# Kernel optimization log

Measured on AMD Instinct MI355X. Metric: run time of the kernel, lower is better.

Reference implementation:

```python
import jax, jax.numpy as jnp
import numpy as np
import math

B, L, C, H = 2, 2048, 768, 12
D = C // H
MAX_SCALE_MUL = math.log(100.0)


def setup_inputs() -> dict:
    key = jax.random.key(0)
    ks = jax.random.split(key, 8)
    std = 0.02
    x = jax.random.normal(ks[0], (B, L, C), dtype=jnp.float32)
    attn_bias = jax.random.normal(ks[1], (1, 1, L, L), dtype=jnp.float32)
    W_qkv = jax.random.normal(ks[2], (3 * C, C), dtype=jnp.float32) * std
    b_qkv = jnp.zeros((3 * C,), dtype=jnp.float32)
    # attn_l2_norm=True: learned per-head log-scale, init log(4)
    scale_mul_log = jnp.full((1, H, 1, 1), math.log(4.0), dtype=jnp.float32)
    W_proj = jax.random.normal(ks[3], (C, C), dtype=jnp.float32) * std
    b_proj = jnp.zeros((C,), dtype=jnp.float32)
    return {"x": x, "attn_bias": attn_bias, "W_qkv": W_qkv, "b_qkv": b_qkv,
            "scale_mul_log": scale_mul_log, "W_proj": W_proj, "b_proj": b_proj}


def _l2norm(t):
    # matches F.normalize(dim=-1, eps=1e-12)
    n = jnp.sqrt(jnp.sum(t * t, axis=-1, keepdims=True))
    return t / jnp.maximum(n, 1e-12)


def reference(x, attn_bias, W_qkv, b_qkv, scale_mul_log, W_proj, b_proj):
    Bx, Lx, Cx = x.shape
    qkv = (x @ W_qkv.T + b_qkv).reshape(Bx, Lx, 3, H, D)
    # -> [3, B, H, L, D]
    qkv = jnp.transpose(qkv, (2, 0, 3, 1, 4))
    q, k, v = qkv[0], qkv[1], qkv[2]
    scale_mul = jnp.exp(jnp.minimum(scale_mul_log, MAX_SCALE_MUL))  # [1,H,1,1]
    q = _l2norm(q) * scale_mul
    k = _l2norm(k)
    # scale = 1 in the l2-norm branch
    attn = jnp.einsum('bhqd,bhkd->bhqk', q, k) + attn_bias
    attn = jax.nn.softmax(attn, axis=-1)
    oup = jnp.einsum('bhqk,bhkd->bhqd', attn, v)          # [B,H,L,D]
    oup = jnp.transpose(oup, (0, 2, 1, 3)).reshape(Bx, Lx, Cx)
    return oup @ W_proj.T + b_proj
```

## Files before the change

kernel.cpp:

```cpp
#include <hip/hip_runtime.h>
#include <math.h>

#define B_ 2
#define L_ 2048
#define C_ 768
#define H_ 12
#define D_ 64
#define M_ (B_ * L_)
#define MAXLOG 4.605170185988091f

typedef __bf16 bf16;
typedef __bf16 bf16x4 __attribute__((ext_vector_type(4)));
typedef __bf16 bf16x8 __attribute__((ext_vector_type(8)));
typedef float  f32x4  __attribute__((ext_vector_type(4)));
typedef short  s16x4  __attribute__((ext_vector_type(4)));

#define SZ_  ((size_t)B_ * H_ * L_ * D_)
#define MC_  ((size_t)M_ * C_)
#define WQ_  ((size_t)3 * C_ * C_)
#define WP_  ((size_t)C_ * C_)

static __device__ __forceinline__ f32x4 mfma16(bf16x4 a, bf16x4 b, f32x4 c) {
#if __has_builtin(__builtin_amdgcn_mfma_f32_16x16x16_bf16)
    return __builtin_amdgcn_mfma_f32_16x16x16_bf16(a, b, c, 0, 0, 0);
#elif __has_builtin(__builtin_amdgcn_mfma_f32_16x16x16bf16_1k)
    return __builtin_amdgcn_mfma_f32_16x16x16bf16_1k(*(s16x4*)&a, *(s16x4*)&b, c, 0, 0, 0);
#else
    f32x4 d;
    asm("v_mfma_f32_16x16x16_bf16 %0, %1, %2, %3" : "=v"(d) : "v"(a), "v"(b), "v"(c));
    return d;
#endif
}

__global__ __launch_bounds__(256) void prep(
    const float4* __restrict__ x, const float4* __restrict__ Wq,
    const float4* __restrict__ Wp,
    bf16* __restrict__ xb, bf16* __restrict__ wqb,
    bf16* __restrict__ Wh, bf16* __restrict__ Wl)
{
    const int X4 = (int)(MC_ / 4);
    const int W4 = (int)(WQ_ / 4);
    const int S4 = (int)(WP_ / 4);
    const int total = X4 + W4 + S4;

    const int i0 = blockIdx.x * 256 + threadIdx.x;
    const int stride = gridDim.x * 256;
    for (int i = i0; i < total; i += stride) {
        if (i < X4) {
            const float4 v = x[i];
            bf16x4 o; o[0]=(bf16)v.x; o[1]=(bf16)v.y; o[2]=(bf16)v.z; o[3]=(bf16)v.w;
            *(bf16x4*)&xb[(size_t)i * 4] = o;
        } else if (i < X4 + W4) {
            const int j = i - X4;
            const float4 v = Wq[j];
            bf16x4 o; o[0]=(bf16)v.x; o[1]=(bf16)v.y; o[2]=(bf16)v.z; o[3]=(bf16)v.w;
            *(bf16x4*)&wqb[(size_t)j * 4] = o;
        } else {
            const int j = i - X4 - W4;
            const float4 v = Wp[j];
            bf16x4 h, l;
            h[0]=(bf16)v.x; l[0]=(bf16)(v.x-(float)h[0]);
            h[1]=(bf16)v.y; l[1]=(bf16)(v.y-(float)h[1]);
            h[2]=(bf16)v.z; l[2]=(bf16)(v.z-(float)h[2]);
            h[3]=(bf16)v.w; l[3]=(bf16)(v.w-(float)h[3]);
            *(bf16x4*)&Wh[(size_t)j * 4] = h;
            *(bf16x4*)&Wl[(size_t)j * 4] = l;
        }
    }
}

__global__ __launch_bounds__(256) void qkv_mfma(
    const bf16* __restrict__ A, const bf16* __restrict__ W,
    const float* __restrict__ bias, const float* __restrict__ sml,
    bf16* __restrict__ qb, bf16* __restrict__ kb, bf16* __restrict__ vtb)
{
    __shared__ __align__(16) bf16 As[128][72];
    __shared__ __align__(16) bf16 Bs[64][72];

    const int t    = threadIdx.x;
    const int w    = t >> 6;
    const int lane = t & 63;
    const int quad = lane >> 4;
    const int c    = lane & 15;
    const int m0   = blockIdx.x * 128;
    const int n0   = blockIdx.y * 64;

    const int r0 = t >> 3;
    const int cg = (t & 7) * 8;

    f32x4 acc[2][4];
    #pragma unroll
    for (int mt = 0; mt < 2; ++mt)
        #pragma unroll
        for (int nt = 0; nt < 4; ++nt) acc[mt][nt] = (f32x4){0.f,0.f,0.f,0.f};

    bf16x8 areg[4], breg[2];
    #pragma unroll
    for (int p = 0; p < 4; ++p)
        areg[p] = *(const bf16x8*)&A[(size_t)(m0 + r0 + 32 * p) * C_ + cg];
    #pragma unroll
    for (int p = 0; p < 2; ++p)
        breg[p] = *(const bf16x8*)&W[(size_t)(n0 + r0 + 32 * p) * C_ + cg];

    for (int kt = 0; kt < C_; kt += 64) {
        __syncthreads();
        #pragma unroll
        for (int p = 0; p < 4; ++p) *(bf16x8*)&As[r0 + 32 * p][cg] = areg[p];
        #pragma unroll
        for (int p = 0; p < 2; ++p) *(bf16x8*)&Bs[r0 + 32 * p][cg] = breg[p];

        const int kt2 = kt + 64;
        if (kt2 < C_) {
            #pragma unroll
            for (int p = 0; p < 4; ++p)
                areg[p] = *(const bf16x8*)&A[(size_t)(m0 + r0 + 32 * p) * C_ + kt2 + cg];
            #pragma unroll
            for (int p = 0; p < 2; ++p)
                breg[p] = *(const bf16x8*)&W[(size_t)(n0 + r0 + 32 * p) * C_ + kt2 + cg];
        }
        __syncthreads();

        #pragma unroll
        for (int ks = 0; ks < 2; ++ks) {
            #pragma unroll
            for (int mt = 0; mt < 2; ++mt) {
                const bf16x8 a = *(const bf16x8*)&As[w * 32 + mt * 16 + c][ks * 32 + quad * 8];
                #pragma unroll
                for (int nt = 0; nt < 4; ++nt) {
                    const bf16x8 b = *(const bf16x8*)&Bs[nt * 16 + c][ks * 32 + quad * 8];
                    acc[mt][nt] = __builtin_amdgcn_mfma_f32_16x16x32_bf16(a, b, acc[mt][nt], 0, 0, 0);
                }
            }
        }
    }

    const int three = blockIdx.y / H_;
    const int h     = blockIdx.y % H_;
    const int bidx  = m0 >> 11;
    const int l0    = (m0 & (L_ - 1)) + w * 32;

    if (three < 2) {
        bf16* dst = (three == 0) ? qb : kb;
        const float scale = (three == 0) ? expf(fminf(sml[h], MAXLOG)) : 1.0f;
        #pragma unroll
        for (int mt = 0; mt < 2; ++mt) {
            float val[4][4];
            float ss[4] = {0.f, 0.f, 0.f, 0.f};
            #pragma unroll
            for (int nt = 0; nt < 4; ++nt) {
                const float bb = bias[n0 + nt * 16 + c];
                #pragma unroll
                for (int reg = 0; reg < 4; ++reg) {
                    const float v = acc[mt][nt][reg] + bb;
                    val[nt][reg] = v;
                    ss[reg] += v * v;
                }
            }
            #pragma unroll
            for (int reg = 0; reg < 4; ++reg) {
                float s = ss[reg];
                #pragma unroll
                for (int off = 1; off < 16; off <<= 1) s += __shfl_xor(s, off, 16);
                const float inv = scale / fmaxf(sqrtf(s), 1e-12f);
                const int l = l0 + mt * 16 + quad * 4 + reg;
                #pragma unroll
                for (int nt = 0; nt < 4; ++nt)
                    dst[((size_t)(bidx * H_ + h) * L_ + l) * D_ + nt * 16 + c] =
                        (bf16)(val[nt][reg] * inv);
            }
        }
    } else {
        #pragma unroll
        for (int mt = 0; mt < 2; ++mt)
            #pragma unroll
            for (int nt = 0; nt < 4; ++nt) {
                const int d = nt * 16 + c;
                const float bb = bias[n0 + d];
                const int l = l0 + mt * 16 + quad * 4;
                bf16x4 o;
                #pragma unroll
                for (int reg = 0; reg < 4; ++reg) o[reg] = (bf16)(acc[mt][nt][reg] + bb);
                *(bf16x4*)&vtb[((size_t)(bidx * H_ + h) * D_ + d) * L_ + l] = o;
            }
    }
}

__global__ __launch_bounds__(256, 3) void flash_mfma(
    const bf16* __restrict__ q, const bf16* __restrict__ k,
    const bf16* __restrict__ vt, const float* __restrict__ bias,
    const float* __restrict__ sml,
    bf16* __restrict__ aoh, bf16* __restrict__ aol)
{
    __shared__ __align__(16) bf16 Ks0 [64][72];
    __shared__ __align__(16) bf16 Vts0[64][72];
    __shared__ __align__(16) bf16 Ks1 [64][72];
    __shared__ __align__(16) bf16 Vts1[64][72];

    const int t    = threadIdx.x;
    const int w    = t >> 6;
    const int lane = t & 63;
    const int quad = lane >> 4;
    const int c    = lane & 15;
    const int q0   = blockIdx.x * 64;
    const int bh   = blockIdx.y;
    const int h    = bh % H_;
    const int b    = bh / H_;
    const size_t base  = (size_t)bh * L_ * D_;
    const size_t vbase = (size_t)bh * D_ * L_;
    const int qrow = q0 + w * 16 + c;

    const float FMAX = expf(fminf(sml[h], MAXLOG)) + 8.0f;

    bf16x8 qf[2];
    qf[0] = *(const bf16x8*)&q[base + (size_t)qrow * D_ + quad * 8];
    qf[1] = *(const bf16x8*)&q[base + (size_t)qrow * D_ + 32 + quad * 8];

    const int r0  = t >> 3,         c00 = (t & 7) * 8;
    const int r1  = (t + 256) >> 3, c01 = ((t + 256) & 7) * 8;

    float l_acc = 0.f;
    f32x4 o[4];
    #pragma unroll
    for (int dt = 0; dt < 4; ++dt) o[dt] = (f32x4){0.f, 0.f, 0.f, 0.f};

    bf16x8 kreg[2], vreg[2];
    f32x4  bregA[4], bregB[4];

    kreg[0] = *(const bf16x8*)&k [base  + (size_t)r0 * D_ + c00];
    kreg[1] = *(const bf16x8*)&k [base  + (size_t)r1 * D_ + c01];
    vreg[0] = *(const bf16x8*)&vt[vbase + (size_t)r0 * L_ + c00];
    vreg[1] = *(const bf16x8*)&vt[vbase + (size_t)r1 * L_ + c01];
    #pragma unroll
    for (int s = 0; s < 4; ++s)
        bregA[s] = *(const f32x4*)&bias[(size_t)qrow * L_ + 16 * s + 4 * quad];

    *(bf16x8*)&Ks0 [r0][c00] = kreg[0];
    *(bf16x8*)&Ks0 [r1][c01] = kreg[1];
    *(bf16x8*)&Vts0[r0][c00] = vreg[0];
    *(bf16x8*)&Vts0[r1][c01] = vreg[1];

    kreg[0] = *(const bf16x8*)&k [base  + (size_t)(64 + r0) * D_ + c00];
    kreg[1] = *(const bf16x8*)&k [base  + (size_t)(64 + r1) * D_ + c01];
    vreg[0] = *(const bf16x8*)&vt[vbase + (size_t)r0 * L_ + 64 + c00];
    vreg[1] = *(const bf16x8*)&vt[vbase + (size_t)r1 * L_ + 64 + c01];
    #pragma unroll
    for (int s = 0; s < 4; ++s)
        bregB[s] = *(const f32x4*)&bias[(size_t)qrow * L_ + 64 + 16 * s + 4 * quad];
    __syncthreads();

#define FSTEP(KS_C, VT_C, KS_N, VT_N, BC, IT) do {                               \
    if ((IT) + 1 < 32) {                                                         \
        *(bf16x8*)&KS_N [r0][c00] = kreg[0];                                     \
        *(bf16x8*)&KS_N [r1][c01] = kreg[1];                                     \
        *(bf16x8*)&VT_N [r0][c00] = vreg[0];                                     \
        *(bf16x8*)&VT_N [r1][c01] = vreg[1];                                     \
    }                                                                            \
    f32x4 st[4];                                                                 \
    _Pragma("unroll") for (int s = 0; s < 4; ++s) st[s] = BC[s];                 \
    if ((IT) + 2 < 32) {                                                         \
        const int kp = ((IT) + 2) * 64;                                          \
        kreg[0] = *(const bf16x8*)&k [base  + (size_t)(kp + r0) * D_ + c00];     \
        kreg[1] = *(const bf16x8*)&k [base  + (size_t)(kp + r1) * D_ + c01];     \
        vreg[0] = *(const bf16x8*)&vt[vbase + (size_t)r0 * L_ + kp + c00];       \
        vreg[1] = *(const bf16x8*)&vt[vbase + (size_t)r1 * L_ + kp + c01];       \
        _Pragma("unroll") for (int s = 0; s < 4; ++s)                            \
            BC[s] = *(const f32x4*)&bias[(size_t)qrow * L_ + kp + 16*s + 4*quad];\
    }                                                                            \
    _Pragma("unroll") for (int ks = 0; ks < 2; ++ks)                             \
        _Pragma("unroll") for (int s = 0; s < 4; ++s) {                          \
            const bf16x8 kf = *(const bf16x8*)&KS_C[s*16 + c][ks*32 + quad*8];   \
            st[s] = __builtin_amdgcn_mfma_f32_16x16x32_bf16(kf, qf[ks], st[s], 0, 0, 0); \
        }                                                                        \
    bf16x4 pf[4];                                                                \
    _Pragma("unroll") for (int s = 0; s < 4; ++s)                                \
        _Pragma("unroll") for (int r = 0; r < 4; ++r) {                          \
            const float pv = __expf(st[s][r] - FMAX);                            \
            l_acc += pv;                                                         \
            pf[s][r] = (bf16)pv;                                                 \
        }                                                                        \
    _Pragma("unroll") for (int s = 0; s < 4; ++s)                                \
        _Pragma("unroll") for (int dt = 0; dt < 4; ++dt) {                       \
            const bf16x4 vfr = *(const bf16x4*)&VT_C[dt*16 + c][16*s + 4*quad];  \
            o[dt] = mfma16(vfr, pf[s], o[dt]);                                   \
        }                                                                        \
    __syncthreads();                                                             \
} while (0)

    for (int it = 0; it < 32; it += 2) {
        FSTEP(Ks0, Vts0, Ks1, Vts1, bregA, it);
        FSTEP(Ks1, Vts1, Ks0, Vts0, bregB, it + 1);
    }
#undef FSTEP

    float rs = l_acc;
    rs += __shfl_xor(rs, 16);
    rs += __shfl_xor(rs, 32);
    const float linv = 1.0f / rs;

    const size_t obase = ((size_t)(b * L_ + qrow)) * C_ + h * 64;
    #pragma unroll
    for (int dt = 0; dt < 4; ++dt) {
        bf16x4 hv, lv;
        #pragma unroll
        for (int r = 0; r < 4; ++r) {
            const float v = o[dt][r] * linv;
            hv[r] = (bf16)v;
            lv[r] = (bf16)(v - (float)hv[r]);
        }
        *(bf16x4*)&aoh[obase + dt * 16 + 4 * quad] = hv;
        *(bf16x4*)&aol[obase + dt * 16 + 4 * quad] = lv;
    }
}

__global__ __launch_bounds__(256) void proj_mfma(
    const bf16* __restrict__ Ahg, const bf16* __restrict__ Alg,
    const bf16* __restrict__ Whg, const bf16* __restrict__ Wlg,
    const float* __restrict__ bias, float* __restrict__ outp)
{
    __shared__ __align__(16) bf16 Ah[64][72];
    __shared__ __align__(16) bf16 Al[64][72];
    __shared__ __align__(16) bf16 Bh[64][72];
    __shared__ __align__(16) bf16 Bl[64][72];

    const int t    = threadIdx.x;
    const int w    = t >> 6;
    const int lane = t & 63;
    const int quad = lane >> 4;
    const int c    = lane & 15;
    const int m0   = blockIdx.x * 64;
    const int n0   = blockIdx.y * 64;

    const int r0 = t >> 3;
    const int cg = (t & 7) * 8;

    f32x4 acc[4];
    #pragma unroll
    for (int nt = 0; nt < 4; ++nt) acc[nt] = (f32x4){0.f,0.f,0.f,0.f};

    bf16x8 ahreg[2], alreg[2], bhreg[2], blreg[2];
    #pragma unroll
    for (int p = 0; p < 2; ++p) {
        ahreg[p] = *(const bf16x8*)&Ahg[(size_t)(m0 + r0 + 32 * p) * C_ + cg];
        alreg[p] = *(const bf16x8*)&Alg[(size_t)(m0 + r0 + 32 * p) * C_ + cg];
        bhreg[p] = *(const bf16x8*)&Whg[(size_t)(n0 + r0 + 32 * p) * C_ + cg];
        blreg[p] = *(const bf16x8*)&Wlg[(size_t)(n0 + r0 + 32 * p) * C_ + cg];
    }

    for (int kt = 0; kt < C_; kt += 64) {
        __syncthreads();
        #pragma unroll
        for (int p = 0; p < 2; ++p) {
            *(bf16x8*)&Ah[r0 + 32 * p][cg] = ahreg[p];
            *(bf16x8*)&Al[r0 + 32 * p][cg] = alreg[p];
            *(bf16x8*)&Bh[r0 + 32 * p][cg] = bhreg[p];
            *(bf16x8*)&Bl[r0 + 32 * p][cg] = blreg[p];
        }

        const int kt2 = kt + 64;
        if (kt2 < C_) {
            #pragma unroll
            for (int p = 0; p < 2; ++p) {
                ahreg[p] = *(const bf16x8*)&Ahg[(size_t)(m0 + r0 + 32 * p) * C_ + kt2 + cg];
                alreg[p] = *(const bf16x8*)&Alg[(size_t)(m0 + r0 + 32 * p) * C_ + kt2 + cg];
                bhreg[p] = *(const bf16x8*)&Whg[(size_t)(n0 + r0 + 32 * p) * C_ + kt2 + cg];
                blreg[p] = *(const bf16x8*)&Wlg[(size_t)(n0 + r0 + 32 * p) * C_ + kt2 + cg];
            }
        }
        __syncthreads();

        #pragma unroll
        for (int ks = 0; ks < 2; ++ks) {
            const bf16x8 ah = *(const bf16x8*)&Ah[w * 16 + c][ks * 32 + quad * 8];
            const bf16x8 al = *(const bf16x8*)&Al[w * 16 + c][ks * 32 + quad * 8];
            #pragma unroll
            for (int nt = 0; nt < 4; ++nt) {
                const bf16x8 bh = *(const bf16x8*)&Bh[nt * 16 + c][ks * 32 + quad * 8];
                const bf16x8 bl = *(const bf16x8*)&Bl[nt * 16 + c][ks * 32 + quad * 8];
                acc[nt] = __builtin_amdgcn_mfma_f32_16x16x32_bf16(ah, bh, acc[nt], 0, 0, 0);
                acc[nt] = __builtin_amdgcn_mfma_f32_16x16x32_bf16(ah, bl, acc[nt], 0, 0, 0);
                acc[nt] = __builtin_amdgcn_mfma_f32_16x16x32_bf16(al, bh, acc[nt], 0, 0, 0);
            }
        }
    }

    #pragma unroll
    for (int nt = 0; nt < 4; ++nt) {
        const int col = n0 + nt * 16 + c;
        const float bb = bias[col];
        #pragma unroll
        for (int reg = 0; reg < 4; ++reg) {
            const int row = m0 + w * 16 + quad * 4 + reg;
            outp[(size_t)row * C_ + col] = acc[nt][reg] + bb;
        }
    }
}

extern "C" void kernel_launch(void* const* d_in, const int* in_sizes, int n_in,
                              void* d_out, int out_size, void* d_ws, size_t ws_size,
                              hipStream_t stream)
{
    const float* x         = (const float*)d_in[0];
    const float* attn_bias = (const float*)d_in[1];
    const float* W_qkv     = (const float*)d_in[2];
    const float* b_qkv     = (const float*)d_in[3];
    const float* sml       = (const float*)d_in[4];
    const float* W_proj    = (const float*)d_in[5];
    const float* b_proj    = (const float*)d_in[6];
    float* out = (float*)d_out;

    bf16* qb  = (bf16*)d_ws;
    bf16* kb  = qb  + SZ_;
    bf16* vtb = kb  + SZ_;
    bf16* aoh = vtb + SZ_;
    bf16* aol = aoh + MC_;
    bf16* Wh  = aol + MC_;
    bf16* Wl  = Wh  + WP_;
    bf16* xb  = Wl  + WP_;
    bf16* wqb = xb  + MC_;

    prep<<<2048, 256, 0, stream>>>(
        (const float4*)x, (const float4*)W_qkv, (const float4*)W_proj,
        xb, wqb, Wh, Wl);

    qkv_mfma<<<dim3(M_ / 128, (3 * C_) / 64), 256, 0, stream>>>(
        xb, wqb, b_qkv, sml, qb, kb, vtb);

    flash_mfma<<<dim3(L_ / 64, B_ * H_), 256, 0, stream>>>(
        qb, kb, vtb, attn_bias, sml, aoh, aol);

    proj_mfma<<<dim3(M_ / 64, C_ / 64), 256, 0, stream>>>(
        aoh, aol, Wh, Wl, b_proj, out);
}
```

Baseline: 200.8 us.

## Give each flash wave two query tiles and swizzle the V-transpose shared layout

```diff
diff --git a/kernel.cpp b/kernel.cpp
--- a/kernel.cpp
+++ b/kernel.cpp
@@ -185,16 +185,16 @@
     }
 }
 
-__global__ __launch_bounds__(256, 3) void flash_mfma(
+__global__ __launch_bounds__(128, 2) void flash_mfma(
     const bf16* __restrict__ q, const bf16* __restrict__ k,
     const bf16* __restrict__ vt, const float* __restrict__ bias,
     const float* __restrict__ sml,
     bf16* __restrict__ aoh, bf16* __restrict__ aol)
 {
     __shared__ __align__(16) bf16 Ks0 [64][72];
-    __shared__ __align__(16) bf16 Vts0[64][72];
     __shared__ __align__(16) bf16 Ks1 [64][72];
-    __shared__ __align__(16) bf16 Vts1[64][72];
+    __shared__ __align__(16) bf16 Vts0[64][64];
+    __shared__ __align__(16) bf16 Vts1[64][64];
 
     const int t    = threadIdx.x;
     const int w    = t >> 6;
@@ -207,108 +207,149 @@
     const int b    = bh / H_;
     const size_t base  = (size_t)bh * L_ * D_;
     const size_t vbase = (size_t)bh * D_ * L_;
-    const int qrow = q0 + w * 16 + c;
 
     const float FMAX = expf(fminf(sml[h], MAXLOG)) + 8.0f;
 
-    bf16x8 qf[2];
-    qf[0] = *(const bf16x8*)&q[base + (size_t)qrow * D_ + quad * 8];
-    qf[1] = *(const bf16x8*)&q[base + (size_t)qrow * D_ + 32 + quad * 8];
-
-    const int r0  = t >> 3,         c00 = (t & 7) * 8;
-    const int r1  = (t + 256) >> 3, c01 = ((t + 256) & 7) * 8;
-
-    float l_acc = 0.f;
-    f32x4 o[4];
-    #pragma unroll
-    for (int dt = 0; dt < 4; ++dt) o[dt] = (f32x4){0.f, 0.f, 0.f, 0.f};
-
-    bf16x8 kreg[2], vreg[2];
-    f32x4  bregA[4], bregB[4];
-
-    kreg[0] = *(const bf16x8*)&k [base  + (size_t)r0 * D_ + c00];
-    kreg[1] = *(const bf16x8*)&k [base  + (size_t)r1 * D_ + c01];
-    vreg[0] = *(const bf16x8*)&vt[vbase + (size_t)r0 * L_ + c00];
-    vreg[1] = *(const bf16x8*)&vt[vbase + (size_t)r1 * L_ + c01];
+    int qrow[2];
+    qrow[0] = q0 + w * 32 + c;
+    qrow[1] = qrow[0] + 16;
+
+    bf16x8 qf[2][2];
+    #pragma unroll
+    for (int qt = 0; qt < 2; ++qt)
+        #pragma unroll
+        for (int ks = 0; ks < 2; ++ks)
+            qf[qt][ks] = *(const bf16x8*)&q[base + (size_t)qrow[qt] * D_ + ks * 32 + quad * 8];
+
+    const int kr0 = t >> 3;
+    const int kc0 = (t & 7) * 8;
+    const int vr0 = t >> 4;
+    const int vch = t & 15;
+
+    int vofs[4];
     #pragma unroll
     for (int s = 0; s < 4; ++s)
-        bregA[s] = *(const f32x4*)&bias[(size_t)qrow * L_ + 16 * s + 4 * quad];
-
-    *(bf16x8*)&Ks0 [r0][c00] = kreg[0];
-    *(bf16x8*)&Ks0 [r1][c01] = kreg[1];
-    *(bf16x8*)&Vts0[r0][c00] = vreg[0];
-    *(bf16x8*)&Vts0[r1][c01] = vreg[1];
-
-    kreg[0] = *(const bf16x8*)&k [base  + (size_t)(64 + r0) * D_ + c00];
-    kreg[1] = *(const bf16x8*)&k [base  + (size_t)(64 + r1) * D_ + c01];
-    vreg[0] = *(const bf16x8*)&vt[vbase + (size_t)r0 * L_ + 64 + c00];
-    vreg[1] = *(const bf16x8*)&vt[vbase + (size_t)r1 * L_ + 64 + c01];
-    #pragma unroll
-    for (int s = 0; s < 4; ++s)
-        bregB[s] = *(const f32x4*)&bias[(size_t)qrow * L_ + 64 + 16 * s + 4 * quad];
+        vofs[s] = c * 128 + 8 * ((4 * s + quad) ^ c);
+
+    size_t brow[2];
+    #pragma unroll
+    for (int qt = 0; qt < 2; ++qt)
+        brow[qt] = (size_t)qrow[qt] * L_ + 4 * quad;
+
+    float l_acc[2] = {0.f, 0.f};
+    f32x4 o[2][4];
+    #pragma unroll
+    for (int qt = 0; qt < 2; ++qt)
+        #pragma unroll
+        for (int dt = 0; dt < 4; ++dt) o[qt][dt] = (f32x4){0.f, 0.f, 0.f, 0.f};
+
+    bf16x8 kreg[4];
+    bf16x4 vreg[8];
+    f32x4  bb[2][4];
+
+    #pragma unroll
+    for (int j = 0; j < 4; ++j)
+        kreg[j] = *(const bf16x8*)&k[base + (size_t)(16 * j + kr0) * D_ + kc0];
+    #pragma unroll
+    for (int j = 0; j < 8; ++j)
+        vreg[j] = *(const bf16x4*)&vt[vbase + (size_t)(8 * j + vr0) * L_ + 4 * vch];
+    #pragma unroll
+    for (int qt = 0; qt < 2; ++qt)
+        #pragma unroll
+        for (int s = 0; s < 4; ++s)
+            bb[qt][s] = *(const f32x4*)&bias[brow[qt] + 16 * s];
+
+    #pragma unroll
+    for (int j = 0; j < 4; ++j)
+        *(bf16x8*)&Ks0[16 * j + kr0][kc0] = kreg[j];
+    #pragma unroll
+    for (int j = 0; j < 8; ++j) {
+        const int vr = 8 * j + vr0;
+        *(bf16x4*)&Vts0[vr][4 * (vch ^ (vr & 15))] = vreg[j];
+    }
+
+    #pragma unroll
+    for (int j = 0; j < 4; ++j)
+        kreg[j] = *(const bf16x8*)&k[base + (size_t)(64 + 16 * j + kr0) * D_ + kc0];
+    #pragma unroll
+    for (int j = 0; j < 8; ++j)
+        vreg[j] = *(const bf16x4*)&vt[vbase + (size_t)(8 * j + vr0) * L_ + 64 + 4 * vch];
     __syncthreads();
 
-#define FSTEP(KS_C, VT_C, KS_N, VT_N, BC, IT) do {                               \
+#define FSTEP(KS_C, VT_C, KS_N, VT_N, IT) do {                                   \
     if ((IT) + 1 < 32) {                                                         \
-        *(bf16x8*)&KS_N [r0][c00] = kreg[0];                                     \
-        *(bf16x8*)&KS_N [r1][c01] = kreg[1];                                     \
-        *(bf16x8*)&VT_N [r0][c00] = vreg[0];                                     \
-        *(bf16x8*)&VT_N [r1][c01] = vreg[1];                                     \
+        _Pragma("unroll") for (int j = 0; j < 4; ++j)                            \
+            *(bf16x8*)&KS_N[16 * j + kr0][kc0] = kreg[j];                        \
+        _Pragma("unroll") for (int j = 0; j < 8; ++j) {                          \
+            const int vr = 8 * j + vr0;                                          \
+            *(bf16x4*)&VT_N[vr][4 * (vch ^ (vr & 15))] = vreg[j];                \
+        }                                                                        \
     }                                                                            \
-    f32x4 st[4];                                                                 \
-    _Pragma("unroll") for (int s = 0; s < 4; ++s) st[s] = BC[s];                 \
+    f32x4 st[2][4];                                                              \
+    _Pragma("unroll") for (int qt = 0; qt < 2; ++qt)                             \
+        _Pragma("unroll") for (int s = 0; s < 4; ++s) st[qt][s] = bb[qt][s];     \
     if ((IT) + 2 < 32) {                                                         \
         const int kp = ((IT) + 2) * 64;                                          \
-        kreg[0] = *(const bf16x8*)&k [base  + (size_t)(kp + r0) * D_ + c00];     \
-        kreg[1] = *(const bf16x8*)&k [base  + (size_t)(kp + r1) * D_ + c01];     \
-        vreg[0] = *(const bf16x8*)&vt[vbase + (size_t)r0 * L_ + kp + c00];       \
-        vreg[1] = *(const bf16x8*)&vt[vbase + (size_t)r1 * L_ + kp + c01];       \
-        _Pragma("unroll") for (int s = 0; s < 4; ++s)                            \
-            BC[s] = *(const f32x4*)&bias[(size_t)qrow * L_ + kp + 16*s + 4*quad];\
+        _Pragma("unroll") for (int j = 0; j < 4; ++j)                            \
+            kreg[j] = *(const bf16x8*)&k[base + (size_t)(kp + 16 * j + kr0) * D_ + kc0]; \
+        _Pragma("unroll") for (int j = 0; j < 8; ++j)                            \
+            vreg[j] = *(const bf16x4*)&vt[vbase + (size_t)(8 * j + vr0) * L_ + kp + 4 * vch]; \
+    }                                                                            \
+    if ((IT) + 1 < 32) {                                                         \
+        const int kn = ((IT) + 1) * 64;                                          \
+        _Pragma("unroll") for (int qt = 0; qt < 2; ++qt)                         \
+            _Pragma("unroll") for (int s = 0; s < 4; ++s)                        \
+                bb[qt][s] = *(const f32x4*)&bias[brow[qt] + kn + 16 * s];        \
     }                                                                            \
     _Pragma("unroll") for (int ks = 0; ks < 2; ++ks)                             \
         _Pragma("unroll") for (int s = 0; s < 4; ++s) {                          \
-            const bf16x8 kf = *(const bf16x8*)&KS_C[s*16 + c][ks*32 + quad*8];   \
-            st[s] = __builtin_amdgcn_mfma_f32_16x16x32_bf16(kf, qf[ks], st[s], 0, 0, 0); \
+            const bf16x8 kf = *(const bf16x8*)&KS_C[16 * s + c][32 * ks + 8 * quad]; \
+            _Pragma("unroll") for (int qt = 0; qt < 2; ++qt)                     \
+                st[qt][s] = __builtin_amdgcn_mfma_f32_16x16x32_bf16(kf, qf[qt][ks], st[qt][s], 0, 0, 0); \
         }                                                                        \
-    bf16x4 pf[4];                                                                \
-    _Pragma("unroll") for (int s = 0; s < 4; ++s)                                \
-        _Pragma("unroll") for (int r = 0; r < 4; ++r) {                          \
-            const float pv = __expf(st[s][r] - FMAX);                            \
-            l_acc += pv;                                                         \
-            pf[s][r] = (bf16)pv;                                                 \
-        }                                                                        \
+    bf16x4 pf[2][4];                                                             \
+    _Pragma("unroll") for (int qt = 0; qt < 2; ++qt)                             \
+        _Pragma("unroll") for (int s = 0; s < 4; ++s)                            \
+            _Pragma("unroll") for (int r = 0; r < 4; ++r) {                      \
+                const float pv = __expf(st[qt][s][r] - FMAX);                    \
+                l_acc[qt] += pv;                                                 \
+                pf[qt][s][r] = (bf16)pv;                                         \
+            }                                                                    \
     _Pragma("unroll") for (int s = 0; s < 4; ++s)                                \
         _Pragma("unroll") for (int dt = 0; dt < 4; ++dt) {                       \
-            const bf16x4 vfr = *(const bf16x4*)&VT_C[dt*16 + c][16*s + 4*quad];  \
-            o[dt] = mfma16(vfr, pf[s], o[dt]);                                   \
+            const bf16x4 vfr = *(const bf16x4*)((const char*)&VT_C[0][0] + vofs[s] + dt * 2048); \
+            _Pragma("unroll") for (int qt = 0; qt < 2; ++qt)                     \
+                o[qt][dt] = mfma16(vfr, pf[qt][s], o[qt][dt]);                   \
         }                                                                        \
     __syncthreads();                                                             \
 } while (0)
 
     for (int it = 0; it < 32; it += 2) {
-        FSTEP(Ks0, Vts0, Ks1, Vts1, bregA, it);
-        FSTEP(Ks1, Vts1, Ks0, Vts0, bregB, it + 1);
+        FSTEP(Ks0, Vts0, Ks1, Vts1, it);
+        FSTEP(Ks1, Vts1, Ks0, Vts0, it + 1);
     }
 #undef FSTEP
 
-    float rs = l_acc;
-    rs += __shfl_xor(rs, 16);
-    rs += __shfl_xor(rs, 32);
-    const float linv = 1.0f / rs;
-
-    const size_t obase = ((size_t)(b * L_ + qrow)) * C_ + h * 64;
-    #pragma unroll
-    for (int dt = 0; dt < 4; ++dt) {
-        bf16x4 hv, lv;
-        #pragma unroll
-        for (int r = 0; r < 4; ++r) {
-            const float v = o[dt][r] * linv;
-            hv[r] = (bf16)v;
-            lv[r] = (bf16)(v - (float)hv[r]);
-        }
-        *(bf16x4*)&aoh[obase + dt * 16 + 4 * quad] = hv;
-        *(bf16x4*)&aol[obase + dt * 16 + 4 * quad] = lv;
+    #pragma unroll
+    for (int qt = 0; qt < 2; ++qt) {
+        float rs = l_acc[qt];
+        rs += __shfl_xor(rs, 16);
+        rs += __shfl_xor(rs, 32);
+        const float linv = 1.0f / rs;
+
+        const size_t obase = ((size_t)(b * L_ + qrow[qt])) * C_ + h * 64;
+        #pragma unroll
+        for (int dt = 0; dt < 4; ++dt) {
+            bf16x4 hv, lv;
+            #pragma unroll
+            for (int r = 0; r < 4; ++r) {
+                const float v = o[qt][dt][r] * linv;
+                hv[r] = (bf16)v;
+                lv[r] = (bf16)(v - (float)hv[r]);
+            }
+            *(bf16x4*)&aoh[obase + dt * 16 + 4 * quad] = hv;
+            *(bf16x4*)&aol[obase + dt * 16 + 4 * quad] = lv;
+        }
     }
 }
 
@@ -425,7 +466,7 @@
     qkv_mfma<<<dim3(M_ / 128, (3 * C_) / 64), 256, 0, stream>>>(
         xb, wqb, b_qkv, sml, qb, kb, vtb);
 
-    flash_mfma<<<dim3(L_ / 64, B_ * H_), 256, 0, stream>>>(
+    flash_mfma<<<dim3(L_ / 64, B_ * H_), 128, 0, stream>>>(
         qb, kb, vtb, attn_bias, sml, aoh, aol);
 
     proj_mfma<<<dim3(M_ / 64, C_ / 64), 256, 0, stream>>>(
```

Measured after the change: 214.2 us. +6.6%, slower.

## Stage GEMM tiles via direct global-to-LDS loads with XOR-swizzled layout

Applied to the files above, without the earlier changes.

```diff
diff --git a/kernel.cpp b/kernel.cpp
--- a/kernel.cpp
+++ b/kernel.cpp
@@ -29,6 +29,16 @@
     f32x4 d;
     asm("v_mfma_f32_16x16x16_bf16 %0, %1, %2, %3" : "=v"(d) : "v"(a), "v"(b), "v"(c));
     return d;
+#endif
+}
+
+static __device__ __forceinline__ void stage16(const bf16* gsrc, void* ldst) {
+#if __has_builtin(__builtin_amdgcn_global_load_lds)
+    __builtin_amdgcn_global_load_lds(
+        (const __attribute__((address_space(1))) unsigned int*)gsrc,
+        (__attribute__((address_space(3))) unsigned int*)ldst, 16, 0, 0);
+#else
+    *(bf16x8*)ldst = *(const bf16x8*)gsrc;
 #endif
 }
 
@@ -74,8 +84,8 @@
     const float* __restrict__ bias, const float* __restrict__ sml,
     bf16* __restrict__ qb, bf16* __restrict__ kb, bf16* __restrict__ vtb)
 {
-    __shared__ __align__(16) bf16 As[128][72];
-    __shared__ __align__(16) bf16 Bs[64][72];
+    __shared__ __align__(16) bf16 As[128][64];
+    __shared__ __align__(16) bf16 Bs[64][64];
 
     const int t    = threadIdx.x;
     const int w    = t >> 6;
@@ -85,49 +95,39 @@
     const int m0   = blockIdx.x * 128;
     const int n0   = blockIdx.y * 64;
 
-    const int r0 = t >> 3;
-    const int cg = (t & 7) * 8;
+    const int sr = t >> 3;
+    const int sc = t & 7;
+    const int sx = sc ^ (sr & 7);
 
     f32x4 acc[2][4];
     #pragma unroll
     for (int mt = 0; mt < 2; ++mt)
         #pragma unroll
         for (int nt = 0; nt < 4; ++nt) acc[mt][nt] = (f32x4){0.f,0.f,0.f,0.f};
-
-    bf16x8 areg[4], breg[2];
-    #pragma unroll
-    for (int p = 0; p < 4; ++p)
-        areg[p] = *(const bf16x8*)&A[(size_t)(m0 + r0 + 32 * p) * C_ + cg];
-    #pragma unroll
-    for (int p = 0; p < 2; ++p)
-        breg[p] = *(const bf16x8*)&W[(size_t)(n0 + r0 + 32 * p) * C_ + cg];
 
     for (int kt = 0; kt < C_; kt += 64) {
         __syncthreads();
         #pragma unroll
-        for (int p = 0; p < 4; ++p) *(bf16x8*)&As[r0 + 32 * p][cg] = areg[p];
-        #pragma unroll
-        for (int p = 0; p < 2; ++p) *(bf16x8*)&Bs[r0 + 32 * p][cg] = breg[p];
-
-        const int kt2 = kt + 64;
-        if (kt2 < C_) {
-            #pragma unroll
-            for (int p = 0; p < 4; ++p)
-                areg[p] = *(const bf16x8*)&A[(size_t)(m0 + r0 + 32 * p) * C_ + kt2 + cg];
-            #pragma unroll
-            for (int p = 0; p < 2; ++p)
-                breg[p] = *(const bf16x8*)&W[(size_t)(n0 + r0 + 32 * p) * C_ + kt2 + cg];
-        }
+        for (int p = 0; p < 4; ++p)
+            stage16(&A[(size_t)(m0 + 32 * p + sr) * C_ + kt + 8 * sx],
+                    (char*)&As[0][0] + (p * 256 + t) * 16);
+        #pragma unroll
+        for (int p = 0; p < 2; ++p)
+            stage16(&W[(size_t)(n0 + 32 * p + sr) * C_ + kt + 8 * sx],
+                    (char*)&Bs[0][0] + (p * 256 + t) * 16);
         __syncthreads();
 
         #pragma unroll
         for (int ks = 0; ks < 2; ++ks) {
+            const int rchunk = ((4 * ks + quad) ^ (c & 7)) * 16;
             #pragma unroll
             for (int mt = 0; mt < 2; ++mt) {
-                const bf16x8 a = *(const bf16x8*)&As[w * 32 + mt * 16 + c][ks * 32 + quad * 8];
+                const bf16x8 a = *(const bf16x8*)((const char*)&As[0][0]
+                                 + (size_t)(w * 32 + mt * 16 + c) * 128 + rchunk);
                 #pragma unroll
                 for (int nt = 0; nt < 4; ++nt) {
-                    const bf16x8 b = *(const bf16x8*)&Bs[nt * 16 + c][ks * 32 + quad * 8];
+                    const bf16x8 b = *(const bf16x8*)((const char*)&Bs[0][0]
+                                     + (size_t)(nt * 16 + c) * 128 + rchunk);
                     acc[mt][nt] = __builtin_amdgcn_mfma_f32_16x16x32_bf16(a, b, acc[mt][nt], 0, 0, 0);
                 }
             }
@@ -192,8 +192,8 @@
     bf16* __restrict__ aoh, bf16* __restrict__ aol)
 {
     __shared__ __align__(16) bf16 Ks0 [64][72];
+    __shared__ __align__(16) bf16 Ks1 [64][72];
     __shared__ __align__(16) bf16 Vts0[64][72];
-    __shared__ __align__(16) bf16 Ks1 [64][72];
     __shared__ __align__(16) bf16 Vts1[64][72];
 
     const int t    = threadIdx.x;
@@ -218,6 +218,8 @@
     const int r0  = t >> 3,         c00 = (t & 7) * 8;
     const int r1  = (t + 256) >> 3, c01 = ((t + 256) & 7) * 8;
 
+    const size_t brow = (size_t)qrow * L_ + 4 * quad;
+
     float l_acc = 0.f;
     f32x4 o[4];
     #pragma unroll
@@ -232,7 +234,7 @@
     vreg[1] = *(const bf16x8*)&vt[vbase + (size_t)r1 * L_ + c01];
     #pragma unroll
     for (int s = 0; s < 4; ++s)
-        bregA[s] = *(const f32x4*)&bias[(size_t)qrow * L_ + 16 * s + 4 * quad];
+        bregA[s] = *(const f32x4*)&bias[brow + 16 * s];
 
     *(bf16x8*)&Ks0 [r0][c00] = kreg[0];
     *(bf16x8*)&Ks0 [r1][c01] = kreg[1];
@@ -245,7 +247,7 @@
     vreg[1] = *(const bf16x8*)&vt[vbase + (size_t)r1 * L_ + 64 + c01];
     #pragma unroll
     for (int s = 0; s < 4; ++s)
-        bregB[s] = *(const f32x4*)&bias[(size_t)qrow * L_ + 64 + 16 * s + 4 * quad];
+        bregB[s] = *(const f32x4*)&bias[brow + 64 + 16 * s];
     __syncthreads();
 
 #define FSTEP(KS_C, VT_C, KS_N, VT_N, BC, IT) do {                               \
@@ -264,7 +266,7 @@
         vreg[0] = *(const bf16x8*)&vt[vbase + (size_t)r0 * L_ + kp + c00];       \
         vreg[1] = *(const bf16x8*)&vt[vbase + (size_t)r1 * L_ + kp + c01];       \
         _Pragma("unroll") for (int s = 0; s < 4; ++s)                            \
-            BC[s] = *(const f32x4*)&bias[(size_t)qrow * L_ + kp + 16*s + 4*quad];\
+            BC[s] = *(const f32x4*)&bias[brow + kp + 16 * s];                    \
     }                                                                            \
     _Pragma("unroll") for (int ks = 0; ks < 2; ++ks)                             \
         _Pragma("unroll") for (int s = 0; s < 4; ++s) {                          \
@@ -317,10 +319,10 @@
     const bf16* __restrict__ Whg, const bf16* __restrict__ Wlg,
     const float* __restrict__ bias, float* __restrict__ outp)
 {
-    __shared__ __align__(16) bf16 Ah[64][72];
-    __shared__ __align__(16) bf16 Al[64][72];
-    __shared__ __align__(16) bf16 Bh[64][72];
-    __shared__ __align__(16) bf16 Bl[64][72];
+    __shared__ __align__(16) bf16 Ah[64][64];
+    __shared__ __align__(16) bf16 Al[64][64];
+    __shared__ __align__(16) bf16 Bh[64][64];
+    __shared__ __align__(16) bf16 Bl[64][64];
 
     const int t    = threadIdx.x;
     const int w    = t >> 6;
@@ -330,52 +332,41 @@
     const int m0   = blockIdx.x * 64;
     const int n0   = blockIdx.y * 64;
 
-    const int r0 = t >> 3;
-    const int cg = (t & 7) * 8;
+    const int sr = t >> 3;
+    const int sc = t & 7;
+    const int sx = sc ^ (sr & 7);
 
     f32x4 acc[4];
     #pragma unroll
     for (int nt = 0; nt < 4; ++nt) acc[nt] = (f32x4){0.f,0.f,0.f,0.f};
-
-    bf16x8 ahreg[2], alreg[2], bhreg[2], blreg[2];
-    #pragma unroll
-    for (int p = 0; p < 2; ++p) {
-        ahreg[p] = *(const bf16x8*)&Ahg[(size_t)(m0 + r0 + 32 * p) * C_ + cg];
-        alreg[p] = *(const bf16x8*)&Alg[(size_t)(m0 + r0 + 32 * p) * C_ + cg];
-        bhreg[p] = *(const bf16x8*)&Whg[(size_t)(n0 + r0 + 32 * p) * C_ + cg];
-        blreg[p] = *(const bf16x8*)&Wlg[(size_t)(n0 + r0 + 32 * p) * C_ + cg];
-    }
 
     for (int kt = 0; kt < C_; kt += 64) {
         __syncthreads();
         #pragma unroll
         for (int p = 0; p < 2; ++p) {
-            *(bf16x8*)&Ah[r0 + 32 * p][cg] = ahreg[p];
-            *(bf16x8*)&Al[r0 + 32 * p][cg] = alreg[p];
-            *(bf16x8*)&Bh[r0 + 32 * p][cg] = bhreg[p];
-            *(bf16x8*)&Bl[r0 + 32 * p][cg] = blreg[p];
-        }
-
-        const int kt2 = kt + 64;
-        if (kt2 < C_) {
-            #pragma unroll
-            for (int p = 0; p < 2; ++p) {
-                ahreg[p] = *(const bf16x8*)&Ahg[(size_t)(m0 + r0 + 32 * p) * C_ + kt2 + cg];
-                alreg[p] = *(const bf16x8*)&Alg[(size_t)(m0 + r0 + 32 * p) * C_ + kt2 + cg];
-                bhreg[p] = *(const bf16x8*)&Whg[(size_t)(n0 + r0 + 32 * p) * C_ + kt2 + cg];
-                blreg[p] = *(const bf16x8*)&Wlg[(size_t)(n0 + r0 + 32 * p) * C_ + kt2 + cg];
-            }
+            const size_t ga = (size_t)(m0 + 32 * p + sr) * C_ + kt + 8 * sx;
+            const size_t gb = (size_t)(n0 + 32 * p + sr) * C_ + kt + 8 * sx;
+            const int    lo = (p * 256 + t) * 16;
+            stage16(&Ahg[ga], (char*)&Ah[0][0] + lo);
+            stage16(&Alg[ga], (char*)&Al[0][0] + lo);
+            stage16(&Whg[gb], (char*)&Bh[0][0] + lo);
+            stage16(&Wlg[gb], (char*)&Bl[0][0] + lo);
         }
         __syncthreads();
 
         #pragma unroll
         for (int ks = 0; ks < 2; ++ks) {
-            const bf16x8 ah = *(const bf16x8*)&Ah[w * 16 + c][ks * 32 + quad * 8];
-            const bf16x8 al = *(const bf16x8*)&Al[w * 16 + c][ks * 32 + quad * 8];
+            const int rchunk = ((4 * ks + quad) ^ (c & 7)) * 16;
+            const bf16x8 ah = *(const bf16x8*)((const char*)&Ah[0][0]
+                              + (size_t)(w * 16 + c) * 128 + rchunk);
+            const bf16x8 al = *(const bf16x8*)((const char*)&Al[0][0]
+                              + (size_t)(w * 16 + c) * 128 + rchunk);
             #pragma unroll
             for (int nt = 0; nt < 4; ++nt) {
-                const bf16x8 bh = *(const bf16x8*)&Bh[nt * 16 + c][ks * 32 + quad * 8];
-                const bf16x8 bl = *(const bf16x8*)&Bl[nt * 16 + c][ks * 32 + quad * 8];
+                const bf16x8 bh = *(const bf16x8*)((const char*)&Bh[0][0]
+                                  + (size_t)(nt * 16 + c) * 128 + rchunk);
+                const bf16x8 bl = *(const bf16x8*)((const char*)&Bl[0][0]
+                                  + (size_t)(nt * 16 + c) * 128 + rchunk);
                 acc[nt] = __builtin_amdgcn_mfma_f32_16x16x32_bf16(ah, bh, acc[nt], 0, 0, 0);
                 acc[nt] = __builtin_amdgcn_mfma_f32_16x16x32_bf16(ah, bl, acc[nt], 0, 0, 0);
                 acc[nt] = __builtin_amdgcn_mfma_f32_16x16x32_bf16(al, bh, acc[nt], 0, 0, 0);
```

Result: no change. 200.4 us (-0.2%).
